# Kernel optimization log

Measured on AMD Instinct MI355X. Metric: run time of the kernel, lower is better.

Reference implementation:

```python
import jax, jax.numpy as jnp
import numpy as np

# ---- HashGridPlanesEncoder config (hybrid-k-planes) ----
NUM_LEVELS = 16
LEVEL_DIM = 2
BASE_RES = 16
DESIRED_RES = 2048
LOG2_HASHMAP = 19
D = 2  # grid_nd: each plane encoder is a 2D hash grid
N_PTS = 1048576
COO_COMBS = [(0, 1), (0, 2), (1, 2)]
HASH_PRIME_1 = 2654435761  # torch-ngp fast_hash prime for dim 1 (dim 0 prime is 1)


def _level_constants():
    # Mirrors torch-ngp GridEncoder offset/resolution computation.
    pls = 2.0 ** (np.log2(DESIRED_RES / BASE_RES) / (NUM_LEVELS - 1))
    max_params = 2 ** LOG2_HASHMAP
    scales, res, sizes, offs = [], [], [], [0]
    for l in range(NUM_LEVELS):
        s = BASE_RES * pls ** l - 1.0          # kernel: scale = exp2(l*S + H) - 1
        r = int(np.ceil(s)) + 1                # kernel: resolution = ceil(scale) + 1
        p = min(max_params, (r + 1) ** D)      # align_corners=False -> (res+1)^D
        p = int(np.ceil(p / 8) * 8)            # round up to multiple of 8
        scales.append(s); res.append(r); sizes.append(p); offs.append(offs[-1] + p)
    return (np.array(scales, np.float32), np.array(res, np.int64),
            np.array(sizes, np.int64), np.array(offs[:-1], np.int64), offs[-1])


SCALES, RES, SIZES, OFFSETS, TOTAL_PARAMS = _level_constants()
USE_HASH = ((RES + 1) ** D) > SIZES  # static per-level: dense linear index vs spatial hash


def _encode_plane(x2, table):
    """x2: [N,2] coords in [0,1]; table: [TOTAL_PARAMS, LEVEL_DIM]. Returns [N, L*C]."""
    n = x2.shape[0]
    scales = jnp.asarray(SCALES)
    pos = x2[:, None, :] * scales[None, :, None] + 0.5           # [N,L,2] (align_corners=False)
    pg_f = jnp.floor(pos)
    frac = pos - pg_f                                            # [N,L,2]
    pg = pg_f.astype(jnp.uint32)
    corners = jnp.array([[0, 0], [1, 0], [0, 1], [1, 1]], jnp.uint32)  # [4,2]
    cpos = pg[:, :, None, :] + corners[None, None]               # [N,L,4,2]
    cmask = corners.astype(bool)[None, None]                     # [1,1,4,2]
    w = jnp.where(cmask, frac[:, :, None, :], 1.0 - frac[:, :, None, :]).prod(-1)  # [N,L,4]
    stride1 = jnp.asarray((RES + 1).astype(np.uint32))           # [L]
    linear = cpos[..., 0] + cpos[..., 1] * stride1[None, :, None]
    hashed = cpos[..., 0] ^ (cpos[..., 1] * jnp.uint32(HASH_PRIME_1))  # uint32 wrap-around
    idx = jnp.where(jnp.asarray(USE_HASH)[None, :, None], hashed, linear)
    idx = idx % jnp.asarray(SIZES.astype(np.uint32))[None, :, None]
    idx = (idx + jnp.asarray(OFFSETS.astype(np.uint32))[None, :, None]).astype(jnp.int32)
    feats = table[idx]                                           # [N,L,4,C] gather
    out = (w[..., None] * feats).sum(axis=2)                     # [N,L,C] bilinear interp
    return out.reshape(n, NUM_LEVELS * LEVEL_DIM)


def setup_inputs() -> dict:
    key = jax.random.key(0)
    kp, k0, k1, k2 = jax.random.split(key, 4)
    pts = jax.random.uniform(kp, (N_PTS, 3), dtype=jnp.float32)  # coords (treated as in [-1,1] domain)
    std = 1e-4  # GridEncoder init: embeddings.uniform_(-1e-4, 1e-4)
    mk = lambda k: jax.random.uniform(k, (TOTAL_PARAMS, LEVEL_DIM), jnp.float32, -std, std)
    return {"pts": pts, "table_xy": mk(k0), "table_xz": mk(k1), "table_yz": mk(k2)}


def reference(pts, table_xy, table_xz, table_yz):
    # GridEncoder.forward normalizes inputs: (x + bound) / (2*bound), bound=1
    u = (pts + 1.0) * 0.5
    tables = (table_xy, table_xz, table_yz)
    out = _encode_plane(u[:, list(COO_COMBS[0])], tables[0])
    for comb, tab in zip(COO_COMBS[1:], tables[1:]):
        out = out + _encode_plane(u[:, list(comb)], tab)
    return out
```

## Files before the change

kernel.cpp:

```cpp
#include <hip/hip_runtime.h>
#include <hip/hip_fp16.h>
#include <cmath>

#define NLEV 16
#define HASH_START 12
#define HMASK ((1u << 19) - 1u)
#define HASH_PRIME 2654435761u
#define LDS_WORDS 14160

typedef float    f4 __attribute__((ext_vector_type(4)));
typedef unsigned u4 __attribute__((ext_vector_type(4)));

struct LvlC {
  float scale[NLEV];
  unsigned stride[NLEV];
  unsigned offset[NLEV];
};

__device__ __forceinline__ float2 h2f(unsigned u) {
  return __half22float2(__builtin_bit_cast(__half2, u));
}

__global__ __launch_bounds__(256) void k_convert(
    const float2* __restrict__ t0, const float2* __restrict__ t1,
    const float2* __restrict__ t2, unsigned* __restrict__ dst, unsigned total)
{
  unsigned g = blockIdx.x * 256 + threadIdx.x;
  unsigned stp = gridDim.x * 256;
  unsigned tot3 = 3u * total;
  for (unsigned e = g; e < tot3; e += stp) {
    const float2* src; unsigned i = e;
    if (i < total)            { src = t0; }
    else if (i < 2u * total)  { src = t1; i -= total; }
    else                      { src = t2; i -= 2u * total; }
    float2 v = src[i];
    __half2 h = __floats2half2_rn(v.x, v.y);
    __builtin_nontemporal_store(__builtin_bit_cast(unsigned, h), dst + e);
  }
}

__device__ __forceinline__ void hash_row(
    const unsigned* __restrict__ tp, unsigned x0, unsigned hy,
    unsigned& g0, unsigned& g1)
{
  unsigned a0 = (x0 ^ hy) & HMASK;
  if ((x0 & 1u) == 0u) {
    uint2 v = *reinterpret_cast<const uint2*>(tp + (a0 & ~1u));
    bool hi = (a0 & 1u) != 0u;
    g0 = hi ? v.y : v.x;
    g1 = hi ? v.x : v.y;
  } else {
    g0 = tp[a0];
    g1 = tp[((x0 + 1u) ^ hy) & HMASK];
  }
}

__device__ __forceinline__ void issue_dense(
    const unsigned* __restrict__ tab, size_t total, const LvlC& lc, int l0,
    const float* ua, const float* ub, uint2 (&g)[2][3][2])
{
#pragma unroll
  for (int h = 0; h < 2; ++h) {
    const float sc = lc.scale[l0 + h];
    const unsigned st = lc.stride[l0 + h], o = lc.offset[l0 + h];
#pragma unroll
    for (int q = 0; q < 3; ++q) {
      float px = ua[q] * sc + .5f, py = ub[q] * sc + .5f;
      unsigned i00 = (unsigned)floorf(px) + (unsigned)floorf(py) * st + o;
      const unsigned* tp = tab + (size_t)q * total;
      g[h][q][0] = *reinterpret_cast<const uint2*>(tp + i00);
      g[h][q][1] = *reinterpret_cast<const uint2*>(tp + i00 + st);
    }
  }
}

__device__ __forceinline__ void consume_dense(
    const LvlC& lc, int l0, const float* ua, const float* ub,
    const uint2 (&g)[2][3][2], float* res4)
{
#pragma unroll
  for (int h = 0; h < 2; ++h) {
    const float sc = lc.scale[l0 + h];
    float s0 = 0.f, s1 = 0.f;
#pragma unroll
    for (int q = 0; q < 3; ++q) {
      float px = ua[q] * sc + .5f, py = ub[q] * sc + .5f;
      float x = px - floorf(px), y = py - floorf(py);
      float w00 = (1.f - x) * (1.f - y), w10 = x * (1.f - y);
      float w01 = (1.f - x) * y,          w11 = x * y;
      float2 f00 = h2f(g[h][q][0].x), f10 = h2f(g[h][q][0].y);
      float2 f01 = h2f(g[h][q][1].x), f11 = h2f(g[h][q][1].y);
      s0 += w00 * f00.x + w10 * f10.x + w01 * f01.x + w11 * f11.x;
      s1 += w00 * f00.y + w10 * f10.y + w01 * f01.y + w11 * f11.y;
    }
    res4[2 * h + 0] = s0; res4[2 * h + 1] = s1;
  }
}

__device__ __forceinline__ void issue_hash1(
    const unsigned* __restrict__ tab, size_t total, const LvlC& lc, int l,
    const float* ua, const float* ub, unsigned (&g)[3][4])
{
  const float sc = lc.scale[l];
  const unsigned o = lc.offset[l];
#pragma unroll
  for (int q = 0; q < 3; ++q) {
    float px = ua[q] * sc + .5f, py = ub[q] * sc + .5f;
    unsigned x0 = (unsigned)floorf(px), y0 = (unsigned)floorf(py);
    unsigned hy0 = y0 * HASH_PRIME, hy1 = hy0 + HASH_PRIME;
    const unsigned* tp = tab + (size_t)q * total + o;
    hash_row(tp, x0, hy0, g[q][0], g[q][1]);
    hash_row(tp, x0, hy1, g[q][2], g[q][3]);
  }
}

__device__ __forceinline__ void consume_hash1(
    const LvlC& lc, int l, const float* ua, const float* ub,
    const unsigned (&g)[3][4], float* res2)
{
  const float sc = lc.scale[l];
  float s0 = 0.f, s1 = 0.f;
#pragma unroll
  for (int q = 0; q < 3; ++q) {
    float px = ua[q] * sc + .5f, py = ub[q] * sc + .5f;
    float x = px - floorf(px), y = py - floorf(py);
    float w00 = (1.f - x) * (1.f - y), w10 = x * (1.f - y);
    float w01 = (1.f - x) * y,          w11 = x * y;
    float2 f00 = h2f(g[q][0]), f10 = h2f(g[q][1]);
    float2 f01 = h2f(g[q][2]), f11 = h2f(g[q][3]);
    s0 += w00 * f00.x + w10 * f10.x + w01 * f01.x + w11 * f11.x;
    s1 += w00 * f00.y + w10 * f10.y + w01 * f01.y + w11 * f11.y;
  }
  res2[0] = s0; res2[1] = s1;
}

__global__ __launch_bounds__(512) void k_final(
    const float* __restrict__ pts, const unsigned* __restrict__ tab,
    float* __restrict__ out, LvlC lc, unsigned total, int n)
{
  __shared__ unsigned lds[LDS_WORDS];
  int i = blockIdx.x * 512 + threadIdx.x;

  float u0 = (pts[3 * i + 0] + 1.f) * .5f;
  float u1 = (pts[3 * i + 1] + 1.f) * .5f;
  float u2 = (pts[3 * i + 2] + 1.f) * .5f;
  const float ua[3] = {u0, u0, u1}, ub[3] = {u1, u2, u2};

  float res[32];
#pragma unroll
  for (int j = 0; j < 12; ++j) res[j] = 0.f;

  uint2 gd[2][3][2];
  unsigned gh[3][4];

  issue_hash1(tab, total, lc, 12, ua, ub, gh);

#pragma unroll 1
  for (int p = 0; p < 3; ++p) {
    if (p) __syncthreads();
    const u4* src = reinterpret_cast<const u4*>(tab + (size_t)p * total);
    for (unsigned e = threadIdx.x; e < LDS_WORDS / 4; e += 512)
      reinterpret_cast<u4*>(lds)[e] = src[e];
    issue_dense(tab, total, lc, 6 + 2 * p, ua, ub, gd);
    __syncthreads();
#pragma unroll
    for (int l = 0; l < 6; ++l) {
      const float sc = lc.scale[l];
      const unsigned st = lc.stride[l], o = lc.offset[l];
      float px = ua[p] * sc + .5f, py = ub[p] * sc + .5f;
      float fx = floorf(px), fy = floorf(py);
      float x = px - fx, y = py - fy;
      unsigned i00 = (unsigned)fx + (unsigned)fy * st + o;
      float2 f00 = h2f(lds[i00]),      f10 = h2f(lds[i00 + 1]);
      float2 f01 = h2f(lds[i00 + st]), f11 = h2f(lds[i00 + st + 1]);
      float w00 = (1.f - x) * (1.f - y), w10 = x * (1.f - y);
      float w01 = (1.f - x) * y,          w11 = x * y;
      res[2 * l + 0] += w00 * f00.x + w10 * f10.x + w01 * f01.x + w11 * f11.x;
      res[2 * l + 1] += w00 * f00.y + w10 * f10.y + w01 * f01.y + w11 * f11.y;
    }
    consume_dense(lc, 6 + 2 * p, ua, ub, gd, res + 12 + 4 * p);
    consume_hash1(lc, 12 + p, ua, ub, gh, res + 24 + 2 * p);
    if (p < 2) issue_hash1(tab, total, lc, 13 + p, ua, ub, gh);
  }

  issue_hash1(tab, total, lc, 15, ua, ub, gh);
  consume_hash1(lc, 15, ua, ub, gh, res + 30);

  float4* o4 = (float4*)(out + (size_t)i * 32);
#pragma unroll
  for (int j = 0; j < 8; ++j)
    o4[j] = make_float4(res[4 * j], res[4 * j + 1], res[4 * j + 2], res[4 * j + 3]);
}

__global__ __launch_bounds__(256) void k_fallback(
    const float* __restrict__ pts, const float2* __restrict__ txy,
    const float2* __restrict__ txz, const float2* __restrict__ tyz,
    float* __restrict__ out, LvlC lc, int n)
{
  int i = blockIdx.x * 256 + threadIdx.x;
  if (i >= n) return;
  float u0 = (pts[3 * i + 0] + 1.f) * .5f;
  float u1 = (pts[3 * i + 1] + 1.f) * .5f;
  float u2 = (pts[3 * i + 2] + 1.f) * .5f;
  const float ua[3] = {u0, u0, u1}, ub[3] = {u1, u2, u2};
  const float2* tabs[3] = {txy, txz, tyz};
  float acc[32];
#pragma unroll
  for (int j = 0; j < 32; ++j) acc[j] = 0.f;
#pragma unroll
  for (int l = 0; l < NLEV; ++l) {
    const float sc = lc.scale[l];
    const unsigned o = lc.offset[l], s = lc.stride[l];
#pragma unroll
    for (int p = 0; p < 3; ++p) {
      const float2* t = tabs[p];
      float px = ua[p] * sc + .5f, py = ub[p] * sc + .5f;
      float fx = floorf(px), fy = floorf(py);
      float rx = px - fx, ry = py - fy;
      unsigned x0 = (unsigned)fx, y0 = (unsigned)fy;
      float w00 = (1.f - rx) * (1.f - ry), w10 = rx * (1.f - ry);
      float w01 = (1.f - rx) * ry,          w11 = rx * ry;
      float2 f00, f10, f01, f11;
      if (l >= HASH_START) {
        unsigned hy0 = y0 * HASH_PRIME, hy1 = hy0 + HASH_PRIME;
        f00 = t[o + ((x0 ^ hy0) & HMASK)];
        f10 = t[o + (((x0 + 1u) ^ hy0) & HMASK)];
        f01 = t[o + ((x0 ^ hy1) & HMASK)];
        f11 = t[o + (((x0 + 1u) ^ hy1) & HMASK)];
      } else {
        unsigned i00 = x0 + y0 * s;
        float4 r0 = *reinterpret_cast<const float4*>(t + o + i00);
        float4 r1 = *reinterpret_cast<const float4*>(t + o + i00 + s);
        f00 = make_float2(r0.x, r0.y); f10 = make_float2(r0.z, r0.w);
        f01 = make_float2(r1.x, r1.y); f11 = make_float2(r1.z, r1.w);
      }
      acc[2 * l + 0] += w00 * f00.x + w10 * f10.x + w01 * f01.x + w11 * f11.x;
      acc[2 * l + 1] += w00 * f00.y + w10 * f10.y + w01 * f01.y + w11 * f11.y;
    }
  }
  float4* o4 = (float4*)(out + (size_t)i * 32);
#pragma unroll
  for (int j = 0; j < 8; ++j)
    o4[j] = make_float4(acc[4 * j], acc[4 * j + 1], acc[4 * j + 2], acc[4 * j + 3]);
}

static unsigned compute_levels(LvlC* lc)
{
  const double pls = std::pow(2.0, std::log2(2048.0 / 16.0) / 15.0);
  unsigned long long off = 0;
  for (int l = 0; l < NLEV; ++l) {
    double s = 16.0 * std::pow(pls, (double)l) - 1.0;
    lc->scale[l] = (float)s;
    long long r = (long long)std::ceil(s) + 1;
    long long dense = (r + 1) * (r + 1);
    long long sz = dense < (1LL << 19) ? dense : (1LL << 19);
    sz = ((sz + 7) / 8) * 8;
    lc->stride[l] = (unsigned)(r + 1);
    lc->offset[l] = (unsigned)off;
    off += (unsigned long long)sz;
  }
  return (unsigned)off;
}

extern "C" void kernel_launch(void* const* d_in, const int* in_sizes, int n_in,
                              void* d_out, int out_size, void* d_ws, size_t ws_size,
                              hipStream_t stream) {
  const float*  pts = (const float*)d_in[0];
  const float2* txy = (const float2*)d_in[1];
  const float2* txz = (const float2*)d_in[2];
  const float2* tyz = (const float2*)d_in[3];
  float* out = (float*)d_out;
  int n = in_sizes[0] / 3;

  LvlC lc;
  unsigned total = compute_levels(&lc);

  size_t need = (size_t)3 * total * 4;

  bool ok = (n % 512 == 0) && (lc.offset[6] == LDS_WORDS) && (ws_size >= need);
  for (int l = HASH_START; l < NLEV; ++l) {
    unsigned sz = ((l + 1 < NLEV) ? lc.offset[l + 1] : total) - lc.offset[l];
    ok = ok && (sz == (1u << 19));
  }

  int block = 256;
  int grid = (n + block - 1) / block;
  if (!ok) {
    k_fallback<<<grid, block, 0, stream>>>(pts, txy, txz, tyz, out, lc, n);
    return;
  }

  unsigned* tab16 = (unsigned*)d_ws;
  k_convert<<<2048, 256, 0, stream>>>(txy, txz, tyz, tab16, total);
  k_final<<<n / 512, 512, 0, stream>>>(pts, tab16, out, lc, total, n);
}
```

Measured before the change: 373.7 us.

## Split hash levels into dedicated blocks interleaved with LDS-based dense blocks

Replaces the single per-point kernel with a mixed grid. Two of every three blocks handle levels 0-11 (LDS-staged coarse levels plus dense global gathers), and the third handles the four hash levels for two points per thread. The aim is to separate latency-bound random hash gathers from LDS-heavy work, lighten per-thread register pressure, and let hash blocks run without LDS or barriers. It drops the software pipelining of hash loads behind dense work. Hash blocks still reserve LDS because the kernel is shared, which may limit occupancy.

```diff
diff --git a/kernel.cpp b/kernel.cpp
--- a/kernel.cpp
+++ b/kernel.cpp
@@ -55,113 +55,44 @@
   }
 }
 
-__device__ __forceinline__ void issue_dense(
-    const unsigned* __restrict__ tab, size_t total, const LvlC& lc, int l0,
-    const float* ua, const float* ub, uint2 (&g)[2][3][2])
-{
-#pragma unroll
-  for (int h = 0; h < 2; ++h) {
-    const float sc = lc.scale[l0 + h];
-    const unsigned st = lc.stride[l0 + h], o = lc.offset[l0 + h];
-#pragma unroll
-    for (int q = 0; q < 3; ++q) {
-      float px = ua[q] * sc + .5f, py = ub[q] * sc + .5f;
-      unsigned i00 = (unsigned)floorf(px) + (unsigned)floorf(py) * st + o;
-      const unsigned* tp = tab + (size_t)q * total;
-      g[h][q][0] = *reinterpret_cast<const uint2*>(tp + i00);
-      g[h][q][1] = *reinterpret_cast<const uint2*>(tp + i00 + st);
-    }
-  }
-}
-
-__device__ __forceinline__ void consume_dense(
-    const LvlC& lc, int l0, const float* ua, const float* ub,
-    const uint2 (&g)[2][3][2], float* res4)
-{
-#pragma unroll
-  for (int h = 0; h < 2; ++h) {
-    const float sc = lc.scale[l0 + h];
-    float s0 = 0.f, s1 = 0.f;
-#pragma unroll
-    for (int q = 0; q < 3; ++q) {
-      float px = ua[q] * sc + .5f, py = ub[q] * sc + .5f;
-      float x = px - floorf(px), y = py - floorf(py);
-      float w00 = (1.f - x) * (1.f - y), w10 = x * (1.f - y);
-      float w01 = (1.f - x) * y,          w11 = x * y;
-      float2 f00 = h2f(g[h][q][0].x), f10 = h2f(g[h][q][0].y);
-      float2 f01 = h2f(g[h][q][1].x), f11 = h2f(g[h][q][1].y);
-      s0 += w00 * f00.x + w10 * f10.x + w01 * f01.x + w11 * f11.x;
-      s1 += w00 * f00.y + w10 * f10.y + w01 * f01.y + w11 * f11.y;
-    }
-    res4[2 * h + 0] = s0; res4[2 * h + 1] = s1;
-  }
-}
-
-__device__ __forceinline__ void issue_hash1(
-    const unsigned* __restrict__ tab, size_t total, const LvlC& lc, int l,
-    const float* ua, const float* ub, unsigned (&g)[3][4])
-{
-  const float sc = lc.scale[l];
-  const unsigned o = lc.offset[l];
-#pragma unroll
-  for (int q = 0; q < 3; ++q) {
-    float px = ua[q] * sc + .5f, py = ub[q] * sc + .5f;
-    unsigned x0 = (unsigned)floorf(px), y0 = (unsigned)floorf(py);
-    unsigned hy0 = y0 * HASH_PRIME, hy1 = hy0 + HASH_PRIME;
-    const unsigned* tp = tab + (size_t)q * total + o;
-    hash_row(tp, x0, hy0, g[q][0], g[q][1]);
-    hash_row(tp, x0, hy1, g[q][2], g[q][3]);
-  }
-}
-
-__device__ __forceinline__ void consume_hash1(
-    const LvlC& lc, int l, const float* ua, const float* ub,
-    const unsigned (&g)[3][4], float* res2)
-{
-  const float sc = lc.scale[l];
-  float s0 = 0.f, s1 = 0.f;
-#pragma unroll
-  for (int q = 0; q < 3; ++q) {
-    float px = ua[q] * sc + .5f, py = ub[q] * sc + .5f;
-    float x = px - floorf(px), y = py - floorf(py);
-    float w00 = (1.f - x) * (1.f - y), w10 = x * (1.f - y);
-    float w01 = (1.f - x) * y,          w11 = x * y;
-    float2 f00 = h2f(g[q][0]), f10 = h2f(g[q][1]);
-    float2 f01 = h2f(g[q][2]), f11 = h2f(g[q][3]);
-    s0 += w00 * f00.x + w10 * f10.x + w01 * f01.x + w11 * f11.x;
-    s1 += w00 * f00.y + w10 * f10.y + w01 * f01.y + w11 * f11.y;
-  }
-  res2[0] = s0; res2[1] = s1;
-}
-
-__global__ __launch_bounds__(512) void k_final(
+__device__ __forceinline__ void final_block(
+    int fb, int tid, unsigned* lds,
     const float* __restrict__ pts, const unsigned* __restrict__ tab,
-    float* __restrict__ out, LvlC lc, unsigned total, int n)
-{
-  __shared__ unsigned lds[LDS_WORDS];
-  int i = blockIdx.x * 512 + threadIdx.x;
+    float* __restrict__ out, const LvlC& lc, unsigned total)
+{
+  int i = fb * 512 + tid;
 
   float u0 = (pts[3 * i + 0] + 1.f) * .5f;
   float u1 = (pts[3 * i + 1] + 1.f) * .5f;
   float u2 = (pts[3 * i + 2] + 1.f) * .5f;
   const float ua[3] = {u0, u0, u1}, ub[3] = {u1, u2, u2};
 
-  float res[32];
+  float res[24];
 #pragma unroll
   for (int j = 0; j < 12; ++j) res[j] = 0.f;
 
   uint2 gd[2][3][2];
-  unsigned gh[3][4];
-
-  issue_hash1(tab, total, lc, 12, ua, ub, gh);
 
 #pragma unroll 1
   for (int p = 0; p < 3; ++p) {
     if (p) __syncthreads();
     const u4* src = reinterpret_cast<const u4*>(tab + (size_t)p * total);
-    for (unsigned e = threadIdx.x; e < LDS_WORDS / 4; e += 512)
+    for (unsigned e = tid; e < LDS_WORDS / 4; e += 512)
       reinterpret_cast<u4*>(lds)[e] = src[e];
-    issue_dense(tab, total, lc, 6 + 2 * p, ua, ub, gd);
+#pragma unroll
+    for (int h = 0; h < 2; ++h) {
+      const int l = 6 + 2 * p + h;
+      const float sc = lc.scale[l];
+      const unsigned st = lc.stride[l], o = lc.offset[l];
+#pragma unroll
+      for (int q = 0; q < 3; ++q) {
+        float px = ua[q] * sc + .5f, py = ub[q] * sc + .5f;
+        unsigned i00 = (unsigned)floorf(px) + (unsigned)floorf(py) * st + o;
+        const unsigned* tp = tab + (size_t)q * total;
+        gd[h][q][0] = *reinterpret_cast<const uint2*>(tp + i00);
+        gd[h][q][1] = *reinterpret_cast<const uint2*>(tp + i00 + st);
+      }
+    }
     __syncthreads();
 #pragma unroll
     for (int l = 0; l < 6; ++l) {
@@ -178,18 +109,109 @@
       res[2 * l + 0] += w00 * f00.x + w10 * f10.x + w01 * f01.x + w11 * f11.x;
       res[2 * l + 1] += w00 * f00.y + w10 * f10.y + w01 * f01.y + w11 * f11.y;
     }
-    consume_dense(lc, 6 + 2 * p, ua, ub, gd, res + 12 + 4 * p);
-    consume_hash1(lc, 12 + p, ua, ub, gh, res + 24 + 2 * p);
-    if (p < 2) issue_hash1(tab, total, lc, 13 + p, ua, ub, gh);
-  }
-
-  issue_hash1(tab, total, lc, 15, ua, ub, gh);
-  consume_hash1(lc, 15, ua, ub, gh, res + 30);
+#pragma unroll
+    for (int h = 0; h < 2; ++h) {
+      const int l = 6 + 2 * p + h;
+      const float sc = lc.scale[l];
+      float s0 = 0.f, s1 = 0.f;
+#pragma unroll
+      for (int q = 0; q < 3; ++q) {
+        float px = ua[q] * sc + .5f, py = ub[q] * sc + .5f;
+        float x = px - floorf(px), y = py - floorf(py);
+        float w00 = (1.f - x) * (1.f - y), w10 = x * (1.f - y);
+        float w01 = (1.f - x) * y,          w11 = x * y;
+        float2 f00 = h2f(gd[h][q][0].x), f10 = h2f(gd[h][q][0].y);
+        float2 f01 = h2f(gd[h][q][1].x), f11 = h2f(gd[h][q][1].y);
+        s0 += w00 * f00.x + w10 * f10.x + w01 * f01.x + w11 * f11.x;
+        s1 += w00 * f00.y + w10 * f10.y + w01 * f01.y + w11 * f11.y;
+      }
+      res[12 + 4 * p + 2 * h + 0] = s0;
+      res[12 + 4 * p + 2 * h + 1] = s1;
+    }
+  }
 
   float4* o4 = (float4*)(out + (size_t)i * 32);
 #pragma unroll
-  for (int j = 0; j < 8; ++j)
+  for (int j = 0; j < 6; ++j)
     o4[j] = make_float4(res[4 * j], res[4 * j + 1], res[4 * j + 2], res[4 * j + 3]);
+}
+
+__device__ __forceinline__ void hash_block(
+    int hb, int tid,
+    const float* __restrict__ pts, const unsigned* __restrict__ tab,
+    float* __restrict__ out, const LvlC& lc, unsigned total, int half)
+{
+  int t = hb * 512 + tid;
+  const int idx[2] = {t, t + half};
+
+  float ua[2][3], ub[2][3];
+#pragma unroll
+  for (int k = 0; k < 2; ++k) {
+    float u0 = (pts[3 * idx[k] + 0] + 1.f) * .5f;
+    float u1 = (pts[3 * idx[k] + 1] + 1.f) * .5f;
+    float u2 = (pts[3 * idx[k] + 2] + 1.f) * .5f;
+    ua[k][0] = u0; ub[k][0] = u1;
+    ua[k][1] = u0; ub[k][1] = u2;
+    ua[k][2] = u1; ub[k][2] = u2;
+  }
+
+  float acc[2][8];
+
+#pragma unroll 1
+  for (int l = HASH_START; l < NLEV; ++l) {
+    const float sc = lc.scale[l];
+    const unsigned o = lc.offset[l];
+    unsigned g[2][3][4];
+#pragma unroll
+    for (int k = 0; k < 2; ++k)
+#pragma unroll
+      for (int q = 0; q < 3; ++q) {
+        float px = ua[k][q] * sc + .5f, py = ub[k][q] * sc + .5f;
+        unsigned x0 = (unsigned)floorf(px), y0 = (unsigned)floorf(py);
+        unsigned hy0 = y0 * HASH_PRIME, hy1 = hy0 + HASH_PRIME;
+        const unsigned* tp = tab + (size_t)q * total + o;
+        hash_row(tp, x0, hy0, g[k][q][0], g[k][q][1]);
+        hash_row(tp, x0, hy1, g[k][q][2], g[k][q][3]);
+      }
+#pragma unroll
+    for (int k = 0; k < 2; ++k) {
+      float s0 = 0.f, s1 = 0.f;
+#pragma unroll
+      for (int q = 0; q < 3; ++q) {
+        float px = ua[k][q] * sc + .5f, py = ub[k][q] * sc + .5f;
+        float x = px - floorf(px), y = py - floorf(py);
+        float w00 = (1.f - x) * (1.f - y), w10 = x * (1.f - y);
+        float w01 = (1.f - x) * y,          w11 = x * y;
+        float2 f00 = h2f(g[k][q][0]), f10 = h2f(g[k][q][1]);
+        float2 f01 = h2f(g[k][q][2]), f11 = h2f(g[k][q][3]);
+        s0 += w00 * f00.x + w10 * f10.x + w01 * f01.x + w11 * f11.x;
+        s1 += w00 * f00.y + w10 * f10.y + w01 * f01.y + w11 * f11.y;
+      }
+      acc[k][2 * (l - HASH_START) + 0] = s0;
+      acc[k][2 * (l - HASH_START) + 1] = s1;
+    }
+  }
+
+#pragma unroll
+  for (int k = 0; k < 2; ++k) {
+    float4* o4 = (float4*)(out + (size_t)idx[k] * 32 + 24);
+    o4[0] = make_float4(acc[k][0], acc[k][1], acc[k][2], acc[k][3]);
+    o4[1] = make_float4(acc[k][4], acc[k][5], acc[k][6], acc[k][7]);
+  }
+}
+
+__global__ __launch_bounds__(512) void k_mix(
+    const float* __restrict__ pts, const unsigned* __restrict__ tab,
+    float* __restrict__ out, LvlC lc, unsigned total, int n)
+{
+  __shared__ unsigned lds[LDS_WORDS];
+  unsigned bid = blockIdx.x;
+  unsigned grp = bid / 3, r = bid % 3;
+  if (r == 2) {
+    hash_block(grp, threadIdx.x, pts, tab, out, lc, total, n >> 1);
+  } else {
+    final_block(grp * 2 + r, threadIdx.x, lds, pts, tab, out, lc, total);
+  }
 }
 
 __global__ __launch_bounds__(256) void k_fallback(
@@ -277,7 +299,7 @@
 
   size_t need = (size_t)3 * total * 4;
 
-  bool ok = (n % 512 == 0) && (lc.offset[6] == LDS_WORDS) && (ws_size >= need);
+  bool ok = (n % 1024 == 0) && (lc.offset[6] == LDS_WORDS) && (ws_size >= need);
   for (int l = HASH_START; l < NLEV; ++l) {
     unsigned sz = ((l + 1 < NLEV) ? lc.offset[l + 1] : total) - lc.offset[l];
     ok = ok && (sz == (1u << 19));
@@ -292,5 +314,6 @@
 
   unsigned* tab16 = (unsigned*)d_ws;
   k_convert<<<2048, 256, 0, stream>>>(txy, txz, tyz, tab16, total);
-  k_final<<<n / 512, 512, 0, stream>>>(pts, tab16, out, lc, total, n);
-}
+  int nmix = 3 * (n / 1024);
+  k_mix<<<nmix, 512, 0, stream>>>(pts, tab16, out, lc, total, n);
+}
```

Result: slower. 444.6 us (+19.0%).
